# Optimization experiments

Measured on AMD Instinct MI355X. Metric: run time of the kernel, lower is better.

Reference implementation:

```python
import jax, jax.numpy as jnp
import numpy as np


def _perceive(x):
    """Depthwise 3x3 perception: per channel emit (identity, dx, dy), matching
    tf.nn.depthwise_conv2d with kernel repeated along the in-channel axis, so
    output channel ordering is [c0_I, c0_dx, c0_dy, c1_I, ...]."""
    C = x.shape[-1]
    _i = jnp.array([0.0, 1.0, 0.0], dtype=x.dtype)
    I = jnp.outer(_i, _i)
    dx = jnp.outer(jnp.array([1.0, 2.0, 1.0], dtype=x.dtype),
                   jnp.array([-1.0, 0.0, 1.0], dtype=x.dtype)) / 8.0
    dy = dx.T
    base = jnp.stack([I, dx, dy], axis=-1)[:, :, None, :]  # [3,3,1,3]
    kernel = jnp.tile(base, (1, 1, 1, C))                   # [3,3,1,3C]
    # grouped conv with feature_group_count=C == depthwise conv, multiplier 3
    y = jax.lax.conv_general_dilated(
        x, kernel, window_strides=(1, 1), padding='SAME',
        dimension_numbers=('NHWC', 'HWIO', 'NHWC'), feature_group_count=C)
    return y  # [B,H,W,3C]


def setup_inputs() -> dict:
    key = jax.random.key(0)
    ks = jax.random.split(key, 6)
    B, H, W, C = 16, 256, 256, 16
    x = jax.random.normal(ks[0], (B, H, W, C), dtype=jnp.float32)
    # update mask: tf.random.normal(...) <= fire_rate (0.5), per pixel
    update_mask = jax.random.normal(ks[1], (B, H, W, 1), dtype=jnp.float32) <= 0.5
    # 1x1 conv weights (glorot-ish scale). NOTE: the original zero-initializes
    # w3/b3; we use small random values so the op is numerically non-trivial.
    w1 = jax.random.normal(ks[2], (3 * C, 4 * C), dtype=jnp.float32) / np.sqrt(3 * C)
    b1 = jnp.zeros((4 * C,), dtype=jnp.float32)
    w2 = jax.random.normal(ks[3], (4 * C, 2 * C), dtype=jnp.float32) / np.sqrt(4 * C)
    b2 = jnp.zeros((2 * C,), dtype=jnp.float32)
    w3 = jax.random.normal(ks[4], (2 * C, C), dtype=jnp.float32) / np.sqrt(2 * C)
    b3 = jnp.zeros((C,), dtype=jnp.float32)
    return {"x": x, "w1": w1, "b1": b1, "w2": w2, "b2": b2,
            "w3": w3, "b3": b3, "update_mask": update_mask}


def reference(x, w1, b1, w2, b2, w3, b3, update_mask):
    step_size = 1.0
    y = _perceive(x)  # [B,H,W,3C]
    h = jnp.tanh(jnp.einsum('bhwc,cd->bhwd', y, w1) + b1)
    h = jnp.tanh(jnp.einsum('bhwc,cd->bhwd', h, w2) + b2)
    dx = (jnp.einsum('bhwc,cd->bhwd', h, w3) + b3) * step_size
    return x + dx * update_mask.astype(x.dtype)
```

## Files before the change

kernel.cpp:

```cpp
#include <hip/hip_runtime.h>
#include <hip/hip_bf16.h>

typedef unsigned int u32;
typedef unsigned short u16;
typedef unsigned char u8;

typedef float f32x16 __attribute__((ext_vector_type(16)));
typedef short bf16x8 __attribute__((ext_vector_type(8)));

#define OFF_A1  0
#define OFF_A1B 18432
#define OFF_WT2 20480
#define OFF_WT3 25600
#define OFF_B3  27648
#define PREP_N  13840

__global__ void probe_kernel(const u16* __restrict__ w1h,
                             const u32* __restrict__ maskw,
                             u32* __restrict__ flags) {
  __shared__ int sg, su8, sbf;
  if (threadIdx.x == 0) { sg = 0; su8 = 0; sbf = 0; }
  __syncthreads();
  int g = 0;
#pragma unroll
  for (int i = 0; i < 8; ++i) {
    u16 h = w1h[threadIdx.x * 8 + i];
    int e = (h >> 7) & 0xFF;
    if (e >= 0xC0) g++;
  }
  if (g) atomicAdd(&sg, g);
  u32 w = maskw[threadIdx.x];
  bool bytes01 = ((w & 0xFEFEFEFEu) == 0u);
  int bsum = (int)(w & 1u) + (int)((w >> 8) & 1u) +
             (int)((w >> 16) & 1u) + (int)((w >> 24) & 1u);
  if (bytes01 && bsum >= 2) atomicAdd(&su8, 1);
  if (w == 0x3F803F80u || w == 0x00003F80u) atomicAdd(&sbf, 1);
  __syncthreads();
  if (threadIdx.x == 0) {
    flags[0] = (sg == 0) ? 1u : 0u;
    flags[1] = (su8 > 0) ? 1u : ((sbf > 0) ? 2u : 4u);
  }
}

__device__ __forceinline__ float bf2f(u16 h) {
  return __uint_as_float(((u32)h) << 16);
}
__device__ __forceinline__ u16 f2bf(float f) {
  u32 u = __float_as_uint(f);
  return (u16)((u + 0x7FFFu + ((u >> 16) & 1u)) >> 16);
}
__device__ __forceinline__ u32 pkbf(float a, float b) {
  u32 ua = __float_as_uint(a) + 0x8000u;
  u32 ub = __float_as_uint(b) + 0x8000u;
  return __builtin_amdgcn_perm(ub, ua, 0x07060302);
}
__device__ __forceinline__ float rdv(const void* s, int i, bool bf) {
  return bf ? bf2f(((const u16*)s)[i]) : ((const float*)s)[i];
}

__global__ void prep_weights(const void* __restrict__ w1, const void* __restrict__ b1,
                             const void* __restrict__ w2, const void* __restrict__ b2,
                             const void* __restrict__ w3, const void* __restrict__ b3,
                             const u32* __restrict__ flags, u8* __restrict__ Wb) {
  int i = blockIdx.x * 256 + threadIdx.x;
  if (i >= PREP_N) return;
  const bool bf = flags[0] != 0;
  if (i < 9216) {
    int off = i >> 10, rem = i & 1023;
    int mt = rem >> 9, hi = (rem >> 8) & 1, l = (rem >> 3) & 31, k8 = i & 7;
    int ch = mt * 32 + l, k = hi * 8 + k8;
    int oi = off / 3, oj = off % 3;
    const float axv[3] = {1.f, 2.f, 1.f};
    const float bxv[3] = {-1.f, 0.f, 1.f};
    float ci  = (oi == 1 && oj == 1) ? 1.f : 0.f;
    float dxv = axv[oi] * bxv[oj] * 0.125f;
    float dyv = axv[oj] * bxv[oi] * 0.125f;
    float v = ci  * rdv(w1, (3 * k + 0) * 64 + ch, bf)
            + dxv * rdv(w1, (3 * k + 1) * 64 + ch, bf)
            + dyv * rdv(w1, (3 * k + 2) * 64 + ch, bf);
    ((u16*)(Wb + OFF_A1))[i] = f2bf(v);
  } else if (i < 10240) {
    int j = i - 9216;
    int mt = j >> 9, l = (j >> 3) & 31;
    ((u16*)(Wb + OFF_A1B))[j] = f2bf(rdv(b1, mt * 32 + l, bf) * 0.0625f);
  } else if (i < 12800) {
    int j = i - 10240, n = j / 80, k = j - n * 80;
    float v;
    if (k < 64) {
      int s = k >> 4, hh = (k >> 3) & 1, q = (k & 7) >> 1, e = k & 1;
      int c = 32 * (s >> 1) + 8 * (2 * (s & 1) + (q >> 1)) + 4 * hh + 2 * (q & 1) + e;
      v = rdv(w2, c * 32 + n, bf);
    } else {
      v = (k == 64) ? rdv(b2, n, bf) : 0.0f;
    }
    ((u16*)(Wb + OFF_WT2))[j] = f2bf(v);
  } else if (i < 13824) {
    int j = i - 12800, n = j >> 5, k = j & 31;
    float v = 0.0f;
    if (n < 16) {
      int cout = (n & 3) + 4 * ((n >> 3) & 1) + 8 * ((n >> 2) & 1);
      int s = k >> 4, hh = (k >> 3) & 1, q = (k & 7) >> 1, e = k & 1;
      int cin = 8 * (2 * s + (q >> 1)) + 4 * hh + 2 * (q & 1) + e;
      v = rdv(w3, cin * 16 + cout, bf);
    }
    ((u16*)(Wb + OFF_WT3))[j] = f2bf(v);
  } else {
    int j = i - 13824;
    ((float*)(Wb + OFF_B3))[j] = rdv(b3, j, bf);
  }
}

__device__ __forceinline__ float fast_tanh(float x) {
  float e = __expf(2.0f * x);
  float r = __builtin_amdgcn_rcpf(e + 1.0f);
  return fmaf(-2.0f, r, 1.0f);
}

union U4 { uint4 q; u32 u[4]; bf16x8 h; float4 f; };

__device__ __forceinline__ void wave_lds_fence() {
  __builtin_amdgcn_wave_barrier();
  __asm__ __volatile__("s_waitcnt lgkmcnt(0)" ::: "memory");
  __builtin_amdgcn_wave_barrier();
}

#define MFMA(a, b, c) __builtin_amdgcn_mfma_f32_32x32x16_bf16((a), (b), (c), 0, 0, 0)

#define XS_STRIDE 8256
#define SCR_OFF   33024
#define SCR_WAVE  5120
#define LDS_TOTAL 53504

template <bool BF16>
__device__ __forceinline__ void nca_body(const void* __restrict__ xv,
                                         const u8* __restrict__ Wb,
                                         const void* __restrict__ maskv, int mw,
                                         void* __restrict__ outv,
                                         u8* __restrict__ xs) {
  const int tid = threadIdx.x;
  const int l   = tid & 63;
  const int wid = tid >> 6;
  const int l31 = l & 31;
  const int hi  = l >> 5;
  const int img   = blockIdx.x >> 7;
  const int r0    = (blockIdx.x & 127) << 1;

  if (tid < 8) {
    int rr = tid >> 1, side = tid & 1;
    uint4 z = make_uint4(0, 0, 0, 0);
    uint4* d = (uint4*)(xs + rr * XS_STRIDE + (side ? 257 : 0) * 32);
    d[0] = z; d[1] = z;
  }
#pragma unroll
  for (int rr = 0; rr < 4; ++rr) {
    int hr = r0 - 1 + rr;
    bool valid = (hr >= 0) && (hr <= 255);
    if (BF16) {
      const u16* src = (const u16*)xv + ((size_t)(img * 256 + hr) << 12);
#pragma unroll
      for (int s = 0; s < 2; ++s) {
        int c = s * 256 + tid;
        uint4 v = make_uint4(0, 0, 0, 0);
        if (valid) v = *(const uint4*)(src + c * 8);
        *(uint4*)(xs + rr * XS_STRIDE + ((c >> 1) + 1) * 32 + (c & 1) * 16) = v;
      }
    } else {
      const float* src = (const float*)xv + ((size_t)(img * 256 + hr) << 12);
#pragma unroll
      for (int k = 0; k < 4; ++k) {
        int q = k * 256 + tid;
        uint2 w = make_uint2(0, 0);
        if (valid) {
          float4 v = *(const float4*)(src + q * 4);
          w.x = pkbf(v.x, v.y); w.y = pkbf(v.z, v.w);
        }
        *(uint2*)(xs + rr * XS_STRIDE + ((q >> 2) + 1) * 32 + (q & 3) * 8) = w;
      }
    }
  }
  __syncthreads();

  const int sr      = wid >> 1;
  const int colbase = (wid & 1) * 128;
  const int gr      = img * 256 + r0 + sr;
  const int growpix = gr << 8;

  bf16x8 A1b[2];
#pragma unroll
  for (int mt = 0; mt < 2; ++mt) {
    U4 t; t.q = *(const uint4*)(Wb + OFF_A1B + ((mt * 2 + hi) * 32 + l31) * 16);
    A1b[mt] = t.h;
  }
  U4 ones; ones.u[0] = ones.u[1] = ones.u[2] = ones.u[3] = 0x3F803F80u;
  const float* B3f = (const float*)(Wb + OFF_B3);
  float4 b3lo = *(const float4*)(B3f + 8 * hi);
  float4 b3hi4 = *(const float4*)(B3f + 8 * hi + 4);
  u8* scr = xs + SCR_OFF + wid * SCR_WAVE;

#pragma unroll
  for (int tp = 0; tp < 2; ++tp) {
#pragma unroll
    for (int u = 0; u < 2; ++u) {
      const int cb = colbase + (tp * 2 + u) * 32;

      f32x16 c0 = {0,0,0,0,0,0,0,0,0,0,0,0,0,0,0,0};
      f32x16 c1 = {0,0,0,0,0,0,0,0,0,0,0,0,0,0,0,0};
      c0 = MFMA(A1b[0], ones.h, c0);
      c1 = MFMA(A1b[1], ones.h, c1);
#pragma unroll
      for (int off = 0; off < 9; ++off) {
        const int oi = off / 3, oj = off % 3;
        U4 bx; bx.q = *(const uint4*)(xs + (sr + oi) * XS_STRIDE +
                                      (cb + l31 + oj) * 32 + hi * 16);
        U4 a0; a0.q = *(const uint4*)(Wb + OFF_A1 + (((off * 2 + 0) * 2 + hi) * 32 + l31) * 16);
        U4 a1; a1.q = *(const uint4*)(Wb + OFF_A1 + (((off * 2 + 1) * 2 + hi) * 32 + l31) * 16);
        c0 = MFMA(a0.h, bx.h, c0);
        c1 = MFMA(a1.h, bx.h, c1);
      }

      u32 o1[16];
#pragma unroll
      for (int g = 0; g < 4; ++g)
#pragma unroll
        for (int pp = 0; pp < 2; ++pp) {
          o1[g * 2 + pp]     = pkbf(fast_tanh(c0[g * 4 + 2 * pp]), fast_tanh(c0[g * 4 + 2 * pp + 1]));
          o1[8 + g * 2 + pp] = pkbf(fast_tanh(c1[g * 4 + 2 * pp]), fast_tanh(c1[g * 4 + 2 * pp + 1]));
        }

      f32x16 c2 = {0,0,0,0,0,0,0,0,0,0,0,0,0,0,0,0};
#pragma unroll
      for (int s = 0; s < 4; ++s) {
        U4 a2; a2.q = *(const uint4*)(Wb + OFF_WT2 + l31 * 160 + s * 32 + hi * 16);
        U4 bfr; bfr.u[0] = o1[4*s]; bfr.u[1] = o1[4*s+1]; bfr.u[2] = o1[4*s+2]; bfr.u[3] = o1[4*s+3];
        c2 = MFMA(a2.h, bfr.h, c2);
      }
      {
        U4 a2; a2.q = *(const uint4*)(Wb + OFF_WT2 + l31 * 160 + 4 * 32 + hi * 16);
        U4 bb; bb.u[0] = hi ? 0u : 0x00003F80u; bb.u[1] = 0; bb.u[2] = 0; bb.u[3] = 0;
        c2 = MFMA(a2.h, bb.h, c2);
      }
      u32 o2[8];
#pragma unroll
      for (int g = 0; g < 4; ++g)
#pragma unroll
        for (int pp = 0; pp < 2; ++pp)
          o2[g * 2 + pp] = pkbf(fast_tanh(c2[g * 4 + 2 * pp]), fast_tanh(c2[g * 4 + 2 * pp + 1]));

      f32x16 c3 = {0,0,0,0,0,0,0,0,0,0,0,0,0,0,0,0};
#pragma unroll
      for (int s = 0; s < 2; ++s) {
        U4 a3; a3.q = *(const uint4*)(Wb + OFF_WT3 + l31 * 64 + s * 32 + hi * 16);
        U4 bfr; bfr.u[0] = o2[4*s]; bfr.u[1] = o2[4*s+1]; bfr.u[2] = o2[4*s+2]; bfr.u[3] = o2[4*s+3];
        c3 = MFMA(a3.h, bfr.h, c3);
      }

      U4 w0, w1;
      w0.f.x = c3[0] + b3lo.x;  w0.f.y = c3[1] + b3lo.y;
      w0.f.z = c3[2] + b3lo.z;  w0.f.w = c3[3] + b3lo.w;
      w1.f.x = c3[4] + b3hi4.x; w1.f.y = c3[5] + b3hi4.y;
      w1.f.z = c3[6] + b3hi4.z; w1.f.w = c3[7] + b3hi4.w;
      u8* sa = scr + (u * 32 + l31) * 80 + hi * 32;
      *(float4*)(sa) = w0.f;
      *(float4*)(sa + 16) = w1.f;
    }
    wave_lds_fence();

    const int cb2 = colbase + tp * 64;
#pragma unroll
    for (int P = 0; P < 4; ++P) {
      const int px_l = P * 16 + (l >> 2);
      const int qd   = l & 3;
      float4 dx = *(const float4*)(scr + px_l * 80 + qd * 16);
      const int gpx = growpix + cb2 + px_l;
      bool ms;
      if (mw == 1)      ms = ((const u8*)maskv)[gpx] != 0;
      else if (mw == 2) ms = ((const u16*)maskv)[gpx] != 0;
      else              ms = ((const u32*)maskv)[gpx] != 0;
      const float mf = ms ? 1.0f : 0.0f;
      const int e = gpx * 16 + qd * 4;
      if (BF16) {
        uint2 xu = *(const uint2*)((const u16*)xv + e);
        float x0 = bf2f((u16)(xu.x & 0xFFFF)), x1 = bf2f((u16)(xu.x >> 16));
        float x2 = bf2f((u16)(xu.y & 0xFFFF)), x3 = bf2f((u16)(xu.y >> 16));
        float o0 = fmaf(dx.x, mf, x0), o1v = fmaf(dx.y, mf, x1);
        float o2v = fmaf(dx.z, mf, x2), o3v = fmaf(dx.w, mf, x3);
        uint2 w; w.x = pkbf(o0, o1v); w.y = pkbf(o2v, o3v);
        *(uint2*)((u16*)outv + e) = w;
      } else {
        float4 xc = *(const float4*)((const float*)xv + e);
        float4 o;
        o.x = fmaf(dx.x, mf, xc.x); o.y = fmaf(dx.y, mf, xc.y);
        o.z = fmaf(dx.z, mf, xc.z); o.w = fmaf(dx.w, mf, xc.w);
        *(float4*)((float*)outv + e) = o;
      }
    }
    wave_lds_fence();
  }
}

__global__ __launch_bounds__(256, 3) void nca_main(const void* __restrict__ xv,
                                                   const u8* __restrict__ Wb,
                                                   const void* __restrict__ maskv,
                                                   const u32* __restrict__ flags,
                                                   void* __restrict__ outv) {
  __shared__ __align__(16) u8 smem[LDS_TOTAL];
  const bool isbf = flags[0] != 0;
  const int mw = (int)flags[1];
  if (isbf) nca_body<true>(xv, Wb, maskv, mw, outv, smem);
  else      nca_body<false>(xv, Wb, maskv, mw, outv, smem);
}

extern "C" void kernel_launch(void* const* d_in, const int* in_sizes, int n_in,
                              void* d_out, int out_size, void* d_ws, size_t ws_size,
                              hipStream_t stream) {
  u32* flags = (u32*)d_ws;
  u8* Wb = (u8*)d_ws + 64;

  probe_kernel<<<1, 256, 0, stream>>>((const u16*)d_in[1], (const u32*)d_in[7], flags);

  prep_weights<<<(PREP_N + 255) / 256, 256, 0, stream>>>(
      d_in[1], d_in[2], d_in[3], d_in[4], d_in[5], d_in[6], flags, Wb);

  const int pixels = in_sizes[7];
  const int blocks = pixels / 512;
  nca_main<<<blocks, 256, 0, stream>>>(d_in[0], Wb, d_in[7], flags, d_out);
}
```

Before: 215.6 us.

## Process four rows per block with rolling row buffer and register-held weights

Each block now handles four image rows instead of two, staging input rows into a 4-slot ring buffer so each halo row is loaded once per block and the next row is fetched during compute. Layer-2/3 weight fragments are hoisted into registers, and the per-wave dx scratch shrinks by storing bf16 instead of fp32, which cuts LDS so launch bounds allow four blocks per CU. This trades fewer blocks (less parallelism) and extra per-row syncthreads for less redundant halo loading. It also adds a bf16 rounding of dx that was previously kept in fp32.

```diff
diff --git a/kernel.cpp b/kernel.cpp
--- a/kernel.cpp
+++ b/kernel.cpp
@@ -128,8 +128,38 @@
 
 #define XS_STRIDE 8256
 #define SCR_OFF   33024
-#define SCR_WAVE  5120
-#define LDS_TOTAL 53504
+#define SCR_WAVE  1280
+#define LDS_TOTAL 38144
+
+template <bool BF16>
+__device__ __forceinline__ void stage_row(const void* __restrict__ xv,
+                                          u8* __restrict__ xs,
+                                          int img, int row, int tid) {
+  const int slot = row & 3;
+  const bool valid = (row >= 0) && (row <= 255);
+  if (BF16) {
+    const u16* src = (const u16*)xv + ((size_t)((img << 8) + row) << 12);
+#pragma unroll
+    for (int s = 0; s < 2; ++s) {
+      int c = s * 256 + tid;
+      uint4 v = make_uint4(0, 0, 0, 0);
+      if (valid) v = *(const uint4*)(src + c * 8);
+      *(uint4*)(xs + slot * XS_STRIDE + ((c >> 1) + 1) * 32 + (c & 1) * 16) = v;
+    }
+  } else {
+    const float* src = (const float*)xv + ((size_t)((img << 8) + row) << 12);
+#pragma unroll
+    for (int k = 0; k < 4; ++k) {
+      int q = k * 256 + tid;
+      uint2 w = make_uint2(0, 0);
+      if (valid) {
+        float4 v = *(const float4*)(src + q * 4);
+        w.x = pkbf(v.x, v.y); w.y = pkbf(v.z, v.w);
+      }
+      *(uint2*)(xs + slot * XS_STRIDE + ((q >> 2) + 1) * 32 + (q & 3) * 8) = w;
+    }
+  }
+}
 
 template <bool BF16>
 __device__ __forceinline__ void nca_body(const void* __restrict__ xv,
@@ -142,48 +172,18 @@
   const int wid = tid >> 6;
   const int l31 = l & 31;
   const int hi  = l >> 5;
-  const int img   = blockIdx.x >> 7;
-  const int r0    = (blockIdx.x & 127) << 1;
+  const int img = blockIdx.x >> 6;
+  const int r0  = (blockIdx.x & 63) << 2;
 
   if (tid < 8) {
-    int rr = tid >> 1, side = tid & 1;
+    int sl = tid >> 1, side = tid & 1;
     uint4 z = make_uint4(0, 0, 0, 0);
-    uint4* d = (uint4*)(xs + rr * XS_STRIDE + (side ? 257 : 0) * 32);
+    uint4* d = (uint4*)(xs + sl * XS_STRIDE + (side ? 257 : 0) * 32);
     d[0] = z; d[1] = z;
   }
-#pragma unroll
-  for (int rr = 0; rr < 4; ++rr) {
-    int hr = r0 - 1 + rr;
-    bool valid = (hr >= 0) && (hr <= 255);
-    if (BF16) {
-      const u16* src = (const u16*)xv + ((size_t)(img * 256 + hr) << 12);
-#pragma unroll
-      for (int s = 0; s < 2; ++s) {
-        int c = s * 256 + tid;
-        uint4 v = make_uint4(0, 0, 0, 0);
-        if (valid) v = *(const uint4*)(src + c * 8);
-        *(uint4*)(xs + rr * XS_STRIDE + ((c >> 1) + 1) * 32 + (c & 1) * 16) = v;
-      }
-    } else {
-      const float* src = (const float*)xv + ((size_t)(img * 256 + hr) << 12);
-#pragma unroll
-      for (int k = 0; k < 4; ++k) {
-        int q = k * 256 + tid;
-        uint2 w = make_uint2(0, 0);
-        if (valid) {
-          float4 v = *(const float4*)(src + q * 4);
-          w.x = pkbf(v.x, v.y); w.y = pkbf(v.z, v.w);
-        }
-        *(uint2*)(xs + rr * XS_STRIDE + ((q >> 2) + 1) * 32 + (q & 3) * 8) = w;
-      }
-    }
-  }
-  __syncthreads();
-
-  const int sr      = wid >> 1;
-  const int colbase = (wid & 1) * 128;
-  const int gr      = img * 256 + r0 + sr;
-  const int growpix = gr << 8;
+  stage_row<BF16>(xv, xs, img, r0 - 1, tid);
+  stage_row<BF16>(xv, xs, img, r0,     tid);
+  stage_row<BF16>(xv, xs, img, r0 + 1, tid);
 
   bf16x8 A1b[2];
 #pragma unroll
@@ -191,17 +191,34 @@
     U4 t; t.q = *(const uint4*)(Wb + OFF_A1B + ((mt * 2 + hi) * 32 + l31) * 16);
     A1b[mt] = t.h;
   }
+  bf16x8 A2f[5];
+#pragma unroll
+  for (int s = 0; s < 5; ++s) {
+    U4 t; t.q = *(const uint4*)(Wb + OFF_WT2 + l31 * 160 + s * 32 + hi * 16);
+    A2f[s] = t.h;
+  }
+  bf16x8 A3f[2];
+#pragma unroll
+  for (int s = 0; s < 2; ++s) {
+    U4 t; t.q = *(const uint4*)(Wb + OFF_WT3 + l31 * 64 + s * 32 + hi * 16);
+    A3f[s] = t.h;
+  }
   U4 ones; ones.u[0] = ones.u[1] = ones.u[2] = ones.u[3] = 0x3F803F80u;
+  U4 bb;   bb.u[0] = hi ? 0u : 0x00003F80u; bb.u[1] = 0; bb.u[2] = 0; bb.u[3] = 0;
   const float* B3f = (const float*)(Wb + OFF_B3);
-  float4 b3lo = *(const float4*)(B3f + 8 * hi);
-  float4 b3hi4 = *(const float4*)(B3f + 8 * hi + 4);
+  const float4 b3lo  = *(const float4*)(B3f + 8 * hi);
+  const float4 b3hi4 = *(const float4*)(B3f + 8 * hi + 4);
   u8* scr = xs + SCR_OFF + wid * SCR_WAVE;
 
-#pragma unroll
-  for (int tp = 0; tp < 2; ++tp) {
+  for (int it = 0; it < 4; ++it) {
+    __syncthreads();
+    const int rr = r0 + it;
+    if (it < 3) stage_row<BF16>(xv, xs, img, rr + 2, tid);
+    const int growpix = ((img << 8) + rr) << 8;
+
 #pragma unroll
     for (int u = 0; u < 2; ++u) {
-      const int cb = colbase + (tp * 2 + u) * 32;
+      const int cb = wid * 64 + u * 32;
 
       f32x16 c0 = {0,0,0,0,0,0,0,0,0,0,0,0,0,0,0,0};
       f32x16 c1 = {0,0,0,0,0,0,0,0,0,0,0,0,0,0,0,0};
@@ -210,7 +227,7 @@
 #pragma unroll
       for (int off = 0; off < 9; ++off) {
         const int oi = off / 3, oj = off % 3;
-        U4 bx; bx.q = *(const uint4*)(xs + (sr + oi) * XS_STRIDE +
+        U4 bx; bx.q = *(const uint4*)(xs + ((rr - 1 + oi) & 3) * XS_STRIDE +
                                       (cb + l31 + oj) * 32 + hi * 16);
         U4 a0; a0.q = *(const uint4*)(Wb + OFF_A1 + (((off * 2 + 0) * 2 + hi) * 32 + l31) * 16);
         U4 a1; a1.q = *(const uint4*)(Wb + OFF_A1 + (((off * 2 + 1) * 2 + hi) * 32 + l31) * 16);
@@ -230,15 +247,11 @@
       f32x16 c2 = {0,0,0,0,0,0,0,0,0,0,0,0,0,0,0,0};
 #pragma unroll
       for (int s = 0; s < 4; ++s) {
-        U4 a2; a2.q = *(const uint4*)(Wb + OFF_WT2 + l31 * 160 + s * 32 + hi * 16);
         U4 bfr; bfr.u[0] = o1[4*s]; bfr.u[1] = o1[4*s+1]; bfr.u[2] = o1[4*s+2]; bfr.u[3] = o1[4*s+3];
-        c2 = MFMA(a2.h, bfr.h, c2);
-      }
-      {
-        U4 a2; a2.q = *(const uint4*)(Wb + OFF_WT2 + l31 * 160 + 4 * 32 + hi * 16);
-        U4 bb; bb.u[0] = hi ? 0u : 0x00003F80u; bb.u[1] = 0; bb.u[2] = 0; bb.u[3] = 0;
-        c2 = MFMA(a2.h, bb.h, c2);
-      }
+        c2 = MFMA(A2f[s], bfr.h, c2);
+      }
+      c2 = MFMA(A2f[4], bb.h, c2);
+
       u32 o2[8];
 #pragma unroll
       for (int g = 0; g < 4; ++g)
@@ -249,56 +262,57 @@
       f32x16 c3 = {0,0,0,0,0,0,0,0,0,0,0,0,0,0,0,0};
 #pragma unroll
       for (int s = 0; s < 2; ++s) {
-        U4 a3; a3.q = *(const uint4*)(Wb + OFF_WT3 + l31 * 64 + s * 32 + hi * 16);
         U4 bfr; bfr.u[0] = o2[4*s]; bfr.u[1] = o2[4*s+1]; bfr.u[2] = o2[4*s+2]; bfr.u[3] = o2[4*s+3];
-        c3 = MFMA(a3.h, bfr.h, c3);
-      }
-
-      U4 w0, w1;
-      w0.f.x = c3[0] + b3lo.x;  w0.f.y = c3[1] + b3lo.y;
-      w0.f.z = c3[2] + b3lo.z;  w0.f.w = c3[3] + b3lo.w;
-      w1.f.x = c3[4] + b3hi4.x; w1.f.y = c3[5] + b3hi4.y;
-      w1.f.z = c3[6] + b3hi4.z; w1.f.w = c3[7] + b3hi4.w;
-      u8* sa = scr + (u * 32 + l31) * 80 + hi * 32;
-      *(float4*)(sa) = w0.f;
-      *(float4*)(sa + 16) = w1.f;
-    }
-    wave_lds_fence();
-
-    const int cb2 = colbase + tp * 64;
-#pragma unroll
-    for (int P = 0; P < 4; ++P) {
-      const int px_l = P * 16 + (l >> 2);
-      const int qd   = l & 3;
-      float4 dx = *(const float4*)(scr + px_l * 80 + qd * 16);
-      const int gpx = growpix + cb2 + px_l;
-      bool ms;
-      if (mw == 1)      ms = ((const u8*)maskv)[gpx] != 0;
-      else if (mw == 2) ms = ((const u16*)maskv)[gpx] != 0;
-      else              ms = ((const u32*)maskv)[gpx] != 0;
-      const float mf = ms ? 1.0f : 0.0f;
-      const int e = gpx * 16 + qd * 4;
-      if (BF16) {
-        uint2 xu = *(const uint2*)((const u16*)xv + e);
-        float x0 = bf2f((u16)(xu.x & 0xFFFF)), x1 = bf2f((u16)(xu.x >> 16));
-        float x2 = bf2f((u16)(xu.y & 0xFFFF)), x3 = bf2f((u16)(xu.y >> 16));
-        float o0 = fmaf(dx.x, mf, x0), o1v = fmaf(dx.y, mf, x1);
-        float o2v = fmaf(dx.z, mf, x2), o3v = fmaf(dx.w, mf, x3);
-        uint2 w; w.x = pkbf(o0, o1v); w.y = pkbf(o2v, o3v);
-        *(uint2*)((u16*)outv + e) = w;
-      } else {
-        float4 xc = *(const float4*)((const float*)xv + e);
-        float4 o;
-        o.x = fmaf(dx.x, mf, xc.x); o.y = fmaf(dx.y, mf, xc.y);
-        o.z = fmaf(dx.z, mf, xc.z); o.w = fmaf(dx.w, mf, xc.w);
-        *(float4*)((float*)outv + e) = o;
-      }
-    }
-    wave_lds_fence();
-  }
-}
-
-__global__ __launch_bounds__(256, 3) void nca_main(const void* __restrict__ xv,
+        c3 = MFMA(A3f[s], bfr.h, c3);
+      }
+
+      {
+        float d0 = c3[0] + b3lo.x,  d1 = c3[1] + b3lo.y;
+        float d2 = c3[2] + b3lo.z,  d3 = c3[3] + b3lo.w;
+        float d4 = c3[4] + b3hi4.x, d5 = c3[5] + b3hi4.y;
+        float d6 = c3[6] + b3hi4.z, d7 = c3[7] + b3hi4.w;
+        u8* sa = scr + l31 * 40 + hi * 16;
+        *(uint2*)(sa)     = make_uint2(pkbf(d0, d1), pkbf(d2, d3));
+        *(uint2*)(sa + 8) = make_uint2(pkbf(d4, d5), pkbf(d6, d7));
+      }
+      wave_lds_fence();
+
+#pragma unroll
+      for (int P = 0; P < 2; ++P) {
+        const int px_l = P * 16 + (l >> 2);
+        const int qd   = l & 3;
+        uint2 dw = *(const uint2*)(scr + px_l * 40 + qd * 8);
+        float dx0 = bf2f((u16)(dw.x & 0xFFFF)), dx1 = bf2f((u16)(dw.x >> 16));
+        float dx2 = bf2f((u16)(dw.y & 0xFFFF)), dx3 = bf2f((u16)(dw.y >> 16));
+        const int gpx = growpix + cb + px_l;
+        bool ms;
+        if (mw == 1)      ms = ((const u8*)maskv)[gpx] != 0;
+        else if (mw == 2) ms = ((const u16*)maskv)[gpx] != 0;
+        else              ms = ((const u32*)maskv)[gpx] != 0;
+        const float mf = ms ? 1.0f : 0.0f;
+        const int e = gpx * 16 + qd * 4;
+        if (BF16) {
+          uint2 xu = *(const uint2*)((const u16*)xv + e);
+          float x0 = bf2f((u16)(xu.x & 0xFFFF)), x1 = bf2f((u16)(xu.x >> 16));
+          float x2 = bf2f((u16)(xu.y & 0xFFFF)), x3 = bf2f((u16)(xu.y >> 16));
+          float o0 = fmaf(dx0, mf, x0), o1v = fmaf(dx1, mf, x1);
+          float o2v = fmaf(dx2, mf, x2), o3v = fmaf(dx3, mf, x3);
+          uint2 w; w.x = pkbf(o0, o1v); w.y = pkbf(o2v, o3v);
+          *(uint2*)((u16*)outv + e) = w;
+        } else {
+          float4 xc = *(const float4*)((const float*)xv + e);
+          float4 o;
+          o.x = fmaf(dx0, mf, xc.x); o.y = fmaf(dx1, mf, xc.y);
+          o.z = fmaf(dx2, mf, xc.z); o.w = fmaf(dx3, mf, xc.w);
+          *(float4*)((float*)outv + e) = o;
+        }
+      }
+      wave_lds_fence();
+    }
+  }
+}
+
+__global__ __launch_bounds__(256, 4) void nca_main(const void* __restrict__ xv,
                                                    const u8* __restrict__ Wb,
                                                    const void* __restrict__ maskv,
                                                    const u32* __restrict__ flags,
@@ -322,6 +336,6 @@
       d_in[1], d_in[2], d_in[3], d_in[4], d_in[5], d_in[6], flags, Wb);
 
   const int pixels = in_sizes[7];
-  const int blocks = pixels / 512;
+  const int blocks = pixels / 1024;
   nca_main<<<blocks, 256, 0, stream>>>(d_in[0], Wb, d_in[7], flags, d_out);
 }
```

Measured after the change: 258.5 us. +19.9%, slower.
